# Kernel optimization log

Measured on AMD Instinct MI355X. Metric: run time of the kernel, lower is better.

## Reference

```python
import jax, jax.numpy as jnp
from jax import lax
import numpy as np

DIM = 64
NUM_HEADS = 1
HEAD_DIM = DIM // NUM_HEADS
SR = 8
EPS = 1e-5


def setup_inputs() -> dict:
    key = jax.random.key(0)
    ks = jax.random.split(key, 12)
    B, H, W = 8, 128, 128
    N = H * W
    s = 1.0 / np.sqrt(DIM)
    x = jax.random.normal(ks[0], (B, N, DIM), dtype=jnp.float32)
    Wq = jax.random.normal(ks[1], (DIM, DIM), dtype=jnp.float32) * s
    bq = jnp.zeros((DIM,), jnp.float32)
    Wk = jax.random.normal(ks[2], (DIM, DIM), dtype=jnp.float32) * s
    bk = jnp.zeros((DIM,), jnp.float32)
    Wv = jax.random.normal(ks[3], (DIM, DIM), dtype=jnp.float32) * s
    bv = jnp.zeros((DIM,), jnp.float32)
    # Conv2D kernel in HWIO layout (Keras default), kernel=stride=SR, padding VALID
    Wsr = jax.random.normal(ks[4], (SR, SR, DIM, DIM), dtype=jnp.float32) * (1.0 / np.sqrt(SR * SR * DIM))
    bsr = jnp.zeros((DIM,), jnp.float32)
    gamma = jnp.ones((DIM,), jnp.float32)
    beta = jnp.zeros((DIM,), jnp.float32)
    Wp = jax.random.normal(ks[5], (DIM, DIM), dtype=jnp.float32) * s
    bp = jnp.zeros((DIM,), jnp.float32)
    return {"x": x, "Wq": Wq, "bq": bq, "Wk": Wk, "bk": bk, "Wv": Wv, "bv": bv,
            "Wsr": Wsr, "bsr": bsr, "gamma": gamma, "beta": beta, "Wp": Wp, "bp": bp,
            "H": H, "W": W}


def reference(x, Wq, bq, Wk, bk, Wv, bv, Wsr, bsr, gamma, beta, Wp, bp, H, W):
    B, N, C = x.shape
    # queries: [B, heads, N, head_dim]
    q = (x @ Wq + bq).reshape(B, N, NUM_HEADS, HEAD_DIM).transpose(0, 2, 1, 3)
    # spatial reduction: strided conv over the token grid, then LayerNorm
    xs = x.reshape(B, H, W, C)
    xs = lax.conv_general_dilated(xs, Wsr, window_strides=(SR, SR), padding='VALID',
                                  dimension_numbers=('NHWC', 'HWIO', 'NHWC')) + bsr
    xs = xs.reshape(B, -1, C)  # [B, Nkv, C], Nkv = (H//SR)*(W//SR)
    mu = jnp.mean(xs, axis=-1, keepdims=True)
    var = jnp.var(xs, axis=-1, keepdims=True)
    xs = (xs - mu) * lax.rsqrt(var + EPS) * gamma + beta
    k = (xs @ Wk + bk).reshape(B, -1, NUM_HEADS, HEAD_DIM).transpose(0, 2, 1, 3)
    v = (xs @ Wv + bv).reshape(B, -1, NUM_HEADS, HEAD_DIM).transpose(0, 2, 1, 3)
    scale = jnp.asarray(np.sqrt(HEAD_DIM), x.dtype)
    attn = jnp.einsum('bhqd,bhkd->bhqk', q, k) / scale
    attn = jax.nn.softmax(attn, axis=-1)
    out = jnp.einsum('bhqk,bhkd->bhqd', attn, v)
    out = out.transpose(0, 2, 1, 3).reshape(B, N, NUM_HEADS * HEAD_DIM)
    return out @ Wp + bp
```

## Files before the change

kernel.cpp:

```cpp
#include <hip/hip_runtime.h>

typedef unsigned short u16;
typedef short short8 __attribute__((ext_vector_type(8)));
typedef short short4v __attribute__((ext_vector_type(4)));
typedef float f32x4 __attribute__((ext_vector_type(4)));
typedef float f4 __attribute__((ext_vector_type(4)));

#define MFMA16(a, b, c) __builtin_amdgcn_mfma_f32_16x16x32_bf16(a, b, c, 0, 0, 0)

__device__ inline u16 f2bf(float f) {
    unsigned int v = __builtin_bit_cast(unsigned int, f);
    unsigned int r = (v + 0x7FFFu + ((v >> 16) & 1u)) >> 16;
    return (u16)r;
}

__global__ __launch_bounds__(256) void prep_kernel(
    const float* __restrict__ Wsr, const float* __restrict__ Wq,
    const float* __restrict__ Wp,
    u16* __restrict__ WsrT, u16* __restrict__ WqT, u16* __restrict__ WpT)
{
    const int bid = blockIdx.x;
    const int tid = threadIdx.x;
    __shared__ float sT[64 * 65];
    const float* src;
    u16* dst;
    if (bid < 64)      { src = Wsr + (size_t)bid * 4096; dst = WsrT + (size_t)bid * 4096; }
    else if (bid == 64){ src = Wq;  dst = WqT; }
    else               { src = Wp;  dst = WpT; }
#pragma unroll
    for (int p = 0; p < 4; ++p) {
        int idx = p * 256 + tid;
        int r = idx >> 4, c4 = (idx & 15) * 4;
        f4 v = *(const f4*)(src + r * 64 + c4);
#pragma unroll
        for (int j = 0; j < 4; ++j) sT[r * 65 + c4 + j] = v[j];
    }
    __syncthreads();
#pragma unroll
    for (int p = 0; p < 2; ++p) {
        int idx = p * 256 + tid;
        int co = idx >> 3, g = (idx & 7) * 8;
        short8 o;
#pragma unroll
        for (int j = 0; j < 8; ++j) o[j] = (short)f2bf(sT[(g + j) * 65 + co]);
        *(short8*)(dst + (size_t)co * 64 + g) = o;
    }
}

__global__ __launch_bounds__(256) void conv_partial_kernel(
    const float* __restrict__ x, const u16* __restrict__ WsrT,
    float* __restrict__ partials)
{
    const int mtile  = blockIdx.x & 31;
    const int ksplit = blockIdx.x >> 5;
    const int tid  = threadIdx.x;
    const int wave = tid >> 6;
    const int lane = tid & 63;
    const int l15  = lane & 15;
    const int quad = lane >> 4;

    __shared__ u16 sA[64 * 72];
    __shared__ u16 sB[64 * 72];

    f32x4 acc[4];
#pragma unroll
    for (int nt = 0; nt < 4; ++nt) { acc[nt][0]=0.f; acc[nt][1]=0.f; acc[nt][2]=0.f; acc[nt][3]=0.f; }

    const int token0 = mtile * 64;
    for (int chunk = 0; chunk < 8; ++chunk) {
        const int cell = ksplit * 8 + chunk;
        const int py = cell >> 3, px = cell & 7;
        __syncthreads();
#pragma unroll
        for (int p = 0; p < 4; ++p) {
            int idx = p * 256 + tid;
            int r = idx >> 4, c4 = (idx & 15) * 4;
            int token = token0 + r;
            int b = token >> 8, rm = token & 255;
            int oy = rm >> 4, ox = rm & 15;
            int y = oy * 8 + py, xc = ox * 8 + px;
            f4 xv = *(const f4*)(x + ((size_t)(b * 16384 + y * 128 + xc)) * 64 + c4);
            short4v s;
#pragma unroll
            for (int j = 0; j < 4; ++j) s[j] = (short)f2bf(xv[j]);
            *(short4v*)&sA[r * 72 + c4] = s;
        }
#pragma unroll
        for (int p = 0; p < 2; ++p) {
            int idx = p * 256 + tid;
            int co = idx >> 3, g = (idx & 7) * 8;
            *(short8*)&sB[co * 72 + g] =
                *(const short8*)(WsrT + (size_t)cell * 4096 + co * 64 + g);
        }
        __syncthreads();
#pragma unroll
        for (int ks = 0; ks < 2; ++ks) {
            short8 af = *(const short8*)&sA[(wave * 16 + l15) * 72 + ks * 32 + quad * 8];
#pragma unroll
            for (int nt = 0; nt < 4; ++nt) {
                short8 bf = *(const short8*)&sB[(nt * 16 + l15) * 72 + ks * 32 + quad * 8];
                acc[nt] = MFMA16(af, bf, acc[nt]);
            }
        }
    }
    float* outp = partials + (size_t)ksplit * 131072;
#pragma unroll
    for (int nt = 0; nt < 4; ++nt)
#pragma unroll
        for (int i = 0; i < 4; ++i) {
            int row = token0 + wave * 16 + quad * 4 + i;
            outp[(size_t)row * 64 + nt * 16 + l15] = acc[nt][i];
        }
}

__global__ __launch_bounds__(256) void lnkv_kernel(
    const float* __restrict__ partials, const float* __restrict__ bsr,
    const float* __restrict__ gamma, const float* __restrict__ beta,
    const float* __restrict__ Wk, const float* __restrict__ bk,
    const float* __restrict__ Wv, const float* __restrict__ bv,
    u16* __restrict__ kbuf, u16* __restrict__ vTbuf)
{
    const int wave = threadIdx.x >> 6;
    const int c    = threadIdx.x & 63;
    const int token = blockIdx.x * 4 + wave;

    float acc = 0.f;
#pragma unroll
    for (int s = 0; s < 8; ++s)
        acc += partials[(size_t)s * 131072 + (size_t)token * 64 + c];
    acc += bsr[c];

    float sum = acc, sumsq = acc * acc;
#pragma unroll
    for (int m = 1; m < 64; m <<= 1) {
        sum   += __shfl_xor(sum, m, 64);
        sumsq += __shfl_xor(sumsq, m, 64);
    }
    float mean = sum * (1.f / 64.f);
    float var  = sumsq * (1.f / 64.f) - mean * mean;
    float inv  = rsqrtf(var + 1e-5f);
    float xn   = (acc - mean) * inv * gamma[c] + beta[c];

    __shared__ float sxn[4][64];
    sxn[wave][c] = xn;

    float ka = bk[c], va = bv[c];
#pragma unroll 8
    for (int ci = 0; ci < 64; ++ci) {
        float xv = sxn[wave][ci];
        ka += xv * Wk[ci * 64 + c];
        va += xv * Wv[ci * 64 + c];
    }
    kbuf[(size_t)token * 64 + c] = f2bf(ka);
    int b = token >> 8, t = token & 255;
    vTbuf[(size_t)b * 16384 + c * 256 + t] = f2bf(va);
}

__global__ __launch_bounds__(512) void attn_kernel(
    const float* __restrict__ x, const u16* __restrict__ WqT,
    const float* __restrict__ bq, const u16* __restrict__ WpT,
    const float* __restrict__ bp, const u16* __restrict__ kbuf,
    const u16* __restrict__ vTbuf, float* __restrict__ out)
{
    const int batch = blockIdx.x >> 7;
    const int row0  = (blockIdx.x & 127) * 128;
    const int tid  = threadIdx.x;
    const int wave = tid >> 6;
    const int lane = tid & 63;
    const int l15  = lane & 15;
    const int quad = lane >> 4;

    __shared__ u16 sK[256 * 72];
    __shared__ u16 sV[64 * 264];
    __shared__ u16 sQ[128 * 72];
    __shared__ u16 sWq[64 * 72];
    __shared__ u16 sWp[64 * 72];
    __shared__ u16 sP[8][16 * 72];

#pragma unroll
    for (int p = 0; p < 4; ++p) {
        int idx = p * 512 + tid; int tt = idx >> 3, seg = idx & 7;
        *(short8*)&sK[tt * 72 + seg * 8] =
            *(const short8*)(kbuf + ((size_t)(batch * 256 + tt)) * 64 + seg * 8);
    }
#pragma unroll
    for (int p = 0; p < 4; ++p) {
        int idx = p * 512 + tid; int d = idx >> 5, seg = idx & 31;
        *(short8*)&sV[d * 264 + seg * 8] =
            *(const short8*)(vTbuf + ((size_t)(batch * 64 + d)) * 256 + seg * 8);
    }
#pragma unroll
    for (int p = 0; p < 4; ++p) {
        int idx = p * 512 + tid; int r = idx >> 4, c4 = (idx & 15) * 4;
        f4 xv = *(const f4*)(x + ((size_t)(batch * 16384 + row0 + r)) * 64 + c4);
        short4v s;
#pragma unroll
        for (int j = 0; j < 4; ++j) s[j] = (short)f2bf(xv[j]);
        *(short4v*)&sQ[r * 72 + c4] = s;
    }
    {
        int co = tid >> 3, g = (tid & 7) * 8;
        *(short8*)&sWq[co * 72 + g] = *(const short8*)(WqT + (size_t)co * 64 + g);
        *(short8*)&sWp[co * 72 + g] = *(const short8*)(WpT + (size_t)co * 64 + g);
    }
    __syncthreads();

    {
        f32x4 qacc[4];
#pragma unroll
        for (int nt = 0; nt < 4; ++nt) { qacc[nt][0]=0.f; qacc[nt][1]=0.f; qacc[nt][2]=0.f; qacc[nt][3]=0.f; }
#pragma unroll
        for (int ks = 0; ks < 2; ++ks) {
            short8 af = *(const short8*)&sQ[(wave * 16 + l15) * 72 + ks * 32 + quad * 8];
#pragma unroll
            for (int nt = 0; nt < 4; ++nt) {
                short8 bf = *(const short8*)&sWq[(nt * 16 + l15) * 72 + ks * 32 + quad * 8];
                qacc[nt] = MFMA16(af, bf, qacc[nt]);
            }
        }
#pragma unroll
        for (int nt = 0; nt < 4; ++nt)
#pragma unroll
            for (int i = 0; i < 4; ++i) {
                int r = wave * 16 + quad * 4 + i, cc = nt * 16 + l15;
                float qv = (qacc[nt][i] + bq[cc]) * 0.125f;
                sQ[r * 72 + cc] = f2bf(qv);
            }
    }

    f32x4 s_acc[16];
#pragma unroll
    for (int nt = 0; nt < 16; ++nt) { s_acc[nt][0]=0.f; s_acc[nt][1]=0.f; s_acc[nt][2]=0.f; s_acc[nt][3]=0.f; }
    {
        short8 aq0 = *(const short8*)&sQ[(wave * 16 + l15) * 72 + quad * 8];
        short8 aq1 = *(const short8*)&sQ[(wave * 16 + l15) * 72 + 32 + quad * 8];
#pragma unroll
        for (int nt = 0; nt < 16; ++nt) {
            short8 b0 = *(const short8*)&sK[(nt * 16 + l15) * 72 + quad * 8];
            s_acc[nt] = MFMA16(aq0, b0, s_acc[nt]);
            short8 b1 = *(const short8*)&sK[(nt * 16 + l15) * 72 + 32 + quad * 8];
            s_acc[nt] = MFMA16(aq1, b1, s_acc[nt]);
        }
    }

    float lrow[4];
#pragma unroll
    for (int i = 0; i < 4; ++i) {
        float m = -1e30f;
#pragma unroll
        for (int nt = 0; nt < 16; ++nt) m = fmaxf(m, s_acc[nt][i]);
#pragma unroll
        for (int msk = 1; msk < 16; msk <<= 1) m = fmaxf(m, __shfl_xor(m, msk, 64));
        float l = 0.f;
#pragma unroll
        for (int nt = 0; nt < 16; ++nt) {
            float pexp = __expf(s_acc[nt][i] - m);
            s_acc[nt][i] = pexp;
            l += pexp;
        }
#pragma unroll
        for (int msk = 1; msk < 16; msk <<= 1) l += __shfl_xor(l, msk, 64);
        lrow[i] = l;
    }

    f32x4 o_acc[4];
#pragma unroll
    for (int nt = 0; nt < 4; ++nt) { o_acc[nt][0]=0.f; o_acc[nt][1]=0.f; o_acc[nt][2]=0.f; o_acc[nt][3]=0.f; }
    for (int ch = 0; ch < 4; ++ch) {
#pragma unroll
        for (int t = 0; t < 4; ++t) {
            int nt = ch * 4 + t;
#pragma unroll
            for (int i = 0; i < 4; ++i)
                sP[wave][(quad * 4 + i) * 72 + t * 16 + l15] = f2bf(s_acc[nt][i]);
        }
#pragma unroll
        for (int ks = 0; ks < 2; ++ks) {
            short8 ap = *(const short8*)&sP[wave][l15 * 72 + ks * 32 + quad * 8];
#pragma unroll
            for (int nt = 0; nt < 4; ++nt) {
                short8 bv_ = *(const short8*)&sV[(nt * 16 + l15) * 264 + ch * 64 + ks * 32 + quad * 8];
                o_acc[nt] = MFMA16(ap, bv_, o_acc[nt]);
            }
        }
    }

#pragma unroll
    for (int nt = 0; nt < 4; ++nt)
#pragma unroll
        for (int i = 0; i < 4; ++i) {
            float ov = o_acc[nt][i] * (1.0f / lrow[i]);
            sP[wave][(quad * 4 + i) * 72 + nt * 16 + l15] = f2bf(ov);
        }
    {
        f32x4 f_acc[4];
#pragma unroll
        for (int nt = 0; nt < 4; ++nt) { f_acc[nt][0]=0.f; f_acc[nt][1]=0.f; f_acc[nt][2]=0.f; f_acc[nt][3]=0.f; }
#pragma unroll
        for (int ks = 0; ks < 2; ++ks) {
            short8 ao = *(const short8*)&sP[wave][l15 * 72 + ks * 32 + quad * 8];
#pragma unroll
            for (int nt = 0; nt < 4; ++nt) {
                short8 bf = *(const short8*)&sWp[(nt * 16 + l15) * 72 + ks * 32 + quad * 8];
                f_acc[nt] = MFMA16(ao, bf, f_acc[nt]);
            }
        }
#pragma unroll
        for (int nt = 0; nt < 4; ++nt)
#pragma unroll
            for (int i = 0; i < 4; ++i) {
                int r = row0 + wave * 16 + quad * 4 + i, cc = nt * 16 + l15;
                out[((size_t)batch * 16384 + r) * 64 + cc] = f_acc[nt][i] + bp[cc];
            }
    }
}

extern "C" void kernel_launch(void* const* d_in, const int* in_sizes, int n_in,
                              void* d_out, int out_size, void* d_ws, size_t ws_size,
                              hipStream_t stream) {
    const float* x     = (const float*)d_in[0];
    const float* Wq    = (const float*)d_in[1];
    const float* bq    = (const float*)d_in[2];
    const float* Wk    = (const float*)d_in[3];
    const float* bk    = (const float*)d_in[4];
    const float* Wv    = (const float*)d_in[5];
    const float* bv    = (const float*)d_in[6];
    const float* Wsr   = (const float*)d_in[7];
    const float* bsr   = (const float*)d_in[8];
    const float* gamma = (const float*)d_in[9];
    const float* beta  = (const float*)d_in[10];
    const float* Wp    = (const float*)d_in[11];
    const float* bp    = (const float*)d_in[12];

    char* w = (char*)d_ws;
    float* partials = (float*)w;
    u16* kbuf  = (u16*)(w + 4194304);
    u16* vTbuf = (u16*)(w + 4194304 + 262144);
    u16* WsrT  = (u16*)(w + 4194304 + 524288);
    u16* WqT   = (u16*)(w + 4194304 + 524288 + 524288);
    u16* WpT   = (u16*)(w + 4194304 + 524288 + 524288 + 8192);
    float* out = (float*)d_out;

    prep_kernel<<<66, 256, 0, stream>>>(Wsr, Wq, Wp, WsrT, WqT, WpT);
    conv_partial_kernel<<<256, 256, 0, stream>>>(x, WsrT, partials);
    lnkv_kernel<<<512, 256, 0, stream>>>(partials, bsr, gamma, beta, Wk, bk, Wv, bv, kbuf, vTbuf);
    attn_kernel<<<1024, 512, 0, stream>>>(x, WqT, bq, WpT, bp, kbuf, vTbuf, out);
}
```

Baseline: 152.9 us.

## Use transposed MFMA formulation to keep attention intermediates in registers

Rewrites the attention kernel to compute transposed products with 16x16x16 bf16 MFMAs so that each accumulator's output layout directly matches the next MFMA's B-operand layout. This removes the LDS round trips for Q, P and O, and Q is loaded straight from global memory. Each wave now handles 32 query rows instead of 16, halving the grid and reusing each K/V/weight fragment across two query tiles. The cost is higher register pressure from the 2x16 score tiles and a smaller MFMA K-depth, which doubles the instruction count.

```diff
diff --git a/kernel.cpp b/kernel.cpp
--- a/kernel.cpp
+++ b/kernel.cpp
@@ -7,11 +7,18 @@
 typedef float f4 __attribute__((ext_vector_type(4)));
 
 #define MFMA16(a, b, c) __builtin_amdgcn_mfma_f32_16x16x32_bf16(a, b, c, 0, 0, 0)
+#define MFMA1K(a, b, c) __builtin_amdgcn_mfma_f32_16x16x16bf16_1k(a, b, c, 0, 0, 0)
 
 __device__ inline u16 f2bf(float f) {
     unsigned int v = __builtin_bit_cast(unsigned int, f);
     unsigned int r = (v + 0x7FFFu + ((v >> 16) & 1u)) >> 16;
     return (u16)r;
+}
+__device__ inline short4v pack4(f4 v) {
+    short4v r;
+#pragma unroll
+    for (int j = 0; j < 4; ++j) r[j] = (short)f2bf(v[j]);
+    return r;
 }
 
 __global__ __launch_bounds__(256) void prep_kernel(
@@ -162,8 +169,8 @@
     const float* __restrict__ bp, const u16* __restrict__ kbuf,
     const u16* __restrict__ vTbuf, float* __restrict__ out)
 {
-    const int batch = blockIdx.x >> 7;
-    const int row0  = (blockIdx.x & 127) * 128;
+    const int batch = blockIdx.x >> 6;
+    const int row0  = (blockIdx.x & 63) * 256;
     const int tid  = threadIdx.x;
     const int wave = tid >> 6;
     const int lane = tid & 63;
@@ -172,10 +179,8 @@
 
     __shared__ u16 sK[256 * 72];
     __shared__ u16 sV[64 * 264];
-    __shared__ u16 sQ[128 * 72];
     __shared__ u16 sWq[64 * 72];
     __shared__ u16 sWp[64 * 72];
-    __shared__ u16 sP[8][16 * 72];
 
 #pragma unroll
     for (int p = 0; p < 4; ++p) {
@@ -189,15 +194,6 @@
         *(short8*)&sV[d * 264 + seg * 8] =
             *(const short8*)(vTbuf + ((size_t)(batch * 64 + d)) * 256 + seg * 8);
     }
-#pragma unroll
-    for (int p = 0; p < 4; ++p) {
-        int idx = p * 512 + tid; int r = idx >> 4, c4 = (idx & 15) * 4;
-        f4 xv = *(const f4*)(x + ((size_t)(batch * 16384 + row0 + r)) * 64 + c4);
-        short4v s;
-#pragma unroll
-        for (int j = 0; j < 4; ++j) s[j] = (short)f2bf(xv[j]);
-        *(short4v*)&sQ[r * 72 + c4] = s;
-    }
     {
         int co = tid >> 3, g = (tid & 7) * 8;
         *(short8*)&sWq[co * 72 + g] = *(const short8*)(WqT + (size_t)co * 64 + g);
@@ -205,113 +201,127 @@
     }
     __syncthreads();
 
-    {
-        f32x4 qacc[4];
-#pragma unroll
-        for (int nt = 0; nt < 4; ++nt) { qacc[nt][0]=0.f; qacc[nt][1]=0.f; qacc[nt][2]=0.f; qacc[nt][3]=0.f; }
-#pragma unroll
-        for (int ks = 0; ks < 2; ++ks) {
-            short8 af = *(const short8*)&sQ[(wave * 16 + l15) * 72 + ks * 32 + quad * 8];
-#pragma unroll
-            for (int nt = 0; nt < 4; ++nt) {
-                short8 bf = *(const short8*)&sWq[(nt * 16 + l15) * 72 + ks * 32 + quad * 8];
-                qacc[nt] = MFMA16(af, bf, qacc[nt]);
-            }
-        }
-#pragma unroll
-        for (int nt = 0; nt < 4; ++nt)
-#pragma unroll
-            for (int i = 0; i < 4; ++i) {
-                int r = wave * 16 + quad * 4 + i, cc = nt * 16 + l15;
-                float qv = (qacc[nt][i] + bq[cc]) * 0.125f;
-                sQ[r * 72 + cc] = f2bf(qv);
-            }
-    }
-
-    f32x4 s_acc[16];
-#pragma unroll
-    for (int nt = 0; nt < 16; ++nt) { s_acc[nt][0]=0.f; s_acc[nt][1]=0.f; s_acc[nt][2]=0.f; s_acc[nt][3]=0.f; }
-    {
-        short8 aq0 = *(const short8*)&sQ[(wave * 16 + l15) * 72 + quad * 8];
-        short8 aq1 = *(const short8*)&sQ[(wave * 16 + l15) * 72 + 32 + quad * 8];
-#pragma unroll
-        for (int nt = 0; nt < 16; ++nt) {
-            short8 b0 = *(const short8*)&sK[(nt * 16 + l15) * 72 + quad * 8];
-            s_acc[nt] = MFMA16(aq0, b0, s_acc[nt]);
-            short8 b1 = *(const short8*)&sK[(nt * 16 + l15) * 72 + 32 + quad * 8];
-            s_acc[nt] = MFMA16(aq1, b1, s_acc[nt]);
-        }
-    }
-
-    float lrow[4];
-#pragma unroll
-    for (int i = 0; i < 4; ++i) {
-        float m = -1e30f;
-#pragma unroll
-        for (int nt = 0; nt < 16; ++nt) m = fmaxf(m, s_acc[nt][i]);
-#pragma unroll
-        for (int msk = 1; msk < 16; msk <<= 1) m = fmaxf(m, __shfl_xor(m, msk, 64));
+    const int qbase = row0 + wave * 32;
+
+    f32x4 qT[2][4];
+#pragma unroll
+    for (int qt = 0; qt < 2; ++qt)
+#pragma unroll
+        for (int ct = 0; ct < 4; ++ct) { qT[qt][ct][0]=0.f; qT[qt][ct][1]=0.f; qT[qt][ct][2]=0.f; qT[qt][ct][3]=0.f; }
+#pragma unroll
+    for (int kt = 0; kt < 4; ++kt) {
+        short4v bfr[2];
+#pragma unroll
+        for (int qt = 0; qt < 2; ++qt) {
+            f4 xv = *(const f4*)(x + ((size_t)(batch * 16384 + qbase + qt * 16 + l15)) * 64 + kt * 16 + quad * 4);
+            bfr[qt] = pack4(xv);
+        }
+#pragma unroll
+        for (int ct = 0; ct < 4; ++ct) {
+            short4v a = *(const short4v*)&sWq[(ct * 16 + l15) * 72 + kt * 16 + quad * 4];
+#pragma unroll
+            for (int qt = 0; qt < 2; ++qt) qT[qt][ct] = MFMA1K(a, bfr[qt], qT[qt][ct]);
+        }
+    }
+    short4v qf[2][4];
+#pragma unroll
+    for (int ct = 0; ct < 4; ++ct) {
+        f4 bqv = *(const f4*)(bq + ct * 16 + quad * 4);
+#pragma unroll
+        for (int qt = 0; qt < 2; ++qt) {
+            f4 t;
+#pragma unroll
+            for (int i = 0; i < 4; ++i) t[i] = (qT[qt][ct][i] + bqv[i]) * 0.125f;
+            qf[qt][ct] = pack4(t);
+        }
+    }
+
+    f32x4 st[2][16];
+#pragma unroll
+    for (int qt = 0; qt < 2; ++qt)
+#pragma unroll
+        for (int mt = 0; mt < 16; ++mt) { st[qt][mt][0]=0.f; st[qt][mt][1]=0.f; st[qt][mt][2]=0.f; st[qt][mt][3]=0.f; }
+#pragma unroll
+    for (int mt = 0; mt < 16; ++mt)
+#pragma unroll
+        for (int kt = 0; kt < 4; ++kt) {
+            short4v a = *(const short4v*)&sK[(mt * 16 + l15) * 72 + kt * 16 + quad * 4];
+#pragma unroll
+            for (int qt = 0; qt < 2; ++qt) st[qt][mt] = MFMA1K(a, qf[qt][kt], st[qt][mt]);
+        }
+
+    short4v pf[2][16];
+    float linv[2];
+#pragma unroll
+    for (int qt = 0; qt < 2; ++qt) {
+        float mx = -1e30f;
+#pragma unroll
+        for (int mt = 0; mt < 16; ++mt)
+#pragma unroll
+            for (int i = 0; i < 4; ++i) mx = fmaxf(mx, st[qt][mt][i]);
+        mx = fmaxf(mx, __shfl_xor(mx, 16, 64));
+        mx = fmaxf(mx, __shfl_xor(mx, 32, 64));
         float l = 0.f;
 #pragma unroll
-        for (int nt = 0; nt < 16; ++nt) {
-            float pexp = __expf(s_acc[nt][i] - m);
-            s_acc[nt][i] = pexp;
-            l += pexp;
-        }
-#pragma unroll
-        for (int msk = 1; msk < 16; msk <<= 1) l += __shfl_xor(l, msk, 64);
-        lrow[i] = l;
-    }
-
-    f32x4 o_acc[4];
-#pragma unroll
-    for (int nt = 0; nt < 4; ++nt) { o_acc[nt][0]=0.f; o_acc[nt][1]=0.f; o_acc[nt][2]=0.f; o_acc[nt][3]=0.f; }
-    for (int ch = 0; ch < 4; ++ch) {
-#pragma unroll
-        for (int t = 0; t < 4; ++t) {
-            int nt = ch * 4 + t;
-#pragma unroll
-            for (int i = 0; i < 4; ++i)
-                sP[wave][(quad * 4 + i) * 72 + t * 16 + l15] = f2bf(s_acc[nt][i]);
-        }
-#pragma unroll
-        for (int ks = 0; ks < 2; ++ks) {
-            short8 ap = *(const short8*)&sP[wave][l15 * 72 + ks * 32 + quad * 8];
-#pragma unroll
-            for (int nt = 0; nt < 4; ++nt) {
-                short8 bv_ = *(const short8*)&sV[(nt * 16 + l15) * 264 + ch * 64 + ks * 32 + quad * 8];
-                o_acc[nt] = MFMA16(ap, bv_, o_acc[nt]);
-            }
-        }
-    }
-
-#pragma unroll
-    for (int nt = 0; nt < 4; ++nt)
-#pragma unroll
-        for (int i = 0; i < 4; ++i) {
-            float ov = o_acc[nt][i] * (1.0f / lrow[i]);
-            sP[wave][(quad * 4 + i) * 72 + nt * 16 + l15] = f2bf(ov);
-        }
-    {
-        f32x4 f_acc[4];
-#pragma unroll
-        for (int nt = 0; nt < 4; ++nt) { f_acc[nt][0]=0.f; f_acc[nt][1]=0.f; f_acc[nt][2]=0.f; f_acc[nt][3]=0.f; }
-#pragma unroll
-        for (int ks = 0; ks < 2; ++ks) {
-            short8 ao = *(const short8*)&sP[wave][l15 * 72 + ks * 32 + quad * 8];
-#pragma unroll
-            for (int nt = 0; nt < 4; ++nt) {
-                short8 bf = *(const short8*)&sWp[(nt * 16 + l15) * 72 + ks * 32 + quad * 8];
-                f_acc[nt] = MFMA16(ao, bf, f_acc[nt]);
-            }
-        }
-#pragma unroll
-        for (int nt = 0; nt < 4; ++nt)
-#pragma unroll
-            for (int i = 0; i < 4; ++i) {
-                int r = row0 + wave * 16 + quad * 4 + i, cc = nt * 16 + l15;
-                out[((size_t)batch * 16384 + r) * 64 + cc] = f_acc[nt][i] + bp[cc];
-            }
+        for (int mt = 0; mt < 16; ++mt) {
+            f4 e;
+#pragma unroll
+            for (int i = 0; i < 4; ++i) { e[i] = __expf(st[qt][mt][i] - mx); l += e[i]; }
+            pf[qt][mt] = pack4(e);
+        }
+        l += __shfl_xor(l, 16, 64);
+        l += __shfl_xor(l, 32, 64);
+        linv[qt] = 1.0f / l;
+    }
+
+    f32x4 ot[2][4];
+#pragma unroll
+    for (int qt = 0; qt < 2; ++qt)
+#pragma unroll
+        for (int dt = 0; dt < 4; ++dt) { ot[qt][dt][0]=0.f; ot[qt][dt][1]=0.f; ot[qt][dt][2]=0.f; ot[qt][dt][3]=0.f; }
+#pragma unroll
+    for (int mt = 0; mt < 16; ++mt)
+#pragma unroll
+        for (int dt = 0; dt < 4; ++dt) {
+            short4v a = *(const short4v*)&sV[(dt * 16 + l15) * 264 + mt * 16 + quad * 4];
+#pragma unroll
+            for (int qt = 0; qt < 2; ++qt) ot[qt][dt] = MFMA1K(a, pf[qt][mt], ot[qt][dt]);
+        }
+
+    short4v of[2][4];
+#pragma unroll
+    for (int dt = 0; dt < 4; ++dt)
+#pragma unroll
+        for (int qt = 0; qt < 2; ++qt) {
+            f4 t;
+#pragma unroll
+            for (int i = 0; i < 4; ++i) t[i] = ot[qt][dt][i] * linv[qt];
+            of[qt][dt] = pack4(t);
+        }
+    f32x4 ft[2][4];
+#pragma unroll
+    for (int qt = 0; qt < 2; ++qt)
+#pragma unroll
+        for (int ct = 0; ct < 4; ++ct) { ft[qt][ct][0]=0.f; ft[qt][ct][1]=0.f; ft[qt][ct][2]=0.f; ft[qt][ct][3]=0.f; }
+#pragma unroll
+    for (int kt = 0; kt < 4; ++kt)
+#pragma unroll
+        for (int ct = 0; ct < 4; ++ct) {
+            short4v a = *(const short4v*)&sWp[(ct * 16 + l15) * 72 + kt * 16 + quad * 4];
+#pragma unroll
+            for (int qt = 0; qt < 2; ++qt) ft[qt][ct] = MFMA1K(a, of[qt][kt], ft[qt][ct]);
+        }
+
+#pragma unroll
+    for (int ct = 0; ct < 4; ++ct) {
+        f4 bpv = *(const f4*)(bp + ct * 16 + quad * 4);
+#pragma unroll
+        for (int qt = 0; qt < 2; ++qt) {
+            f4 r;
+#pragma unroll
+            for (int i = 0; i < 4; ++i) r[i] = ft[qt][ct][i] + bpv[i];
+            *(f4*)(out + ((size_t)(batch * 16384 + qbase + qt * 16 + l15)) * 64 + ct * 16 + quad * 4) = r;
+        }
     }
 }
 
@@ -344,5 +354,5 @@
     prep_kernel<<<66, 256, 0, stream>>>(Wsr, Wq, Wp, WsrT, WqT, WpT);
     conv_partial_kernel<<<256, 256, 0, stream>>>(x, WsrT, partials);
     lnkv_kernel<<<512, 256, 0, stream>>>(partials, bsr, gamma, beta, Wk, bk, Wv, bv, kbuf, vTbuf);
-    attn_kernel<<<1024, 512, 0, stream>>>(x, WqT, bq, WpT, bp, kbuf, vTbuf, out);
-}
+    attn_kernel<<<512, 512, 0, stream>>>(x, WqT, bq, WpT, bp, kbuf, vTbuf, out);
+}
```

Result: faster. 148.4 us (-2.9%).
